# Kernel optimization log

Measured on AMD Instinct MI355X. Metric: run time of the kernel, lower is better.

Reference implementation:

```python
import jax, jax.numpy as jnp
import numpy as np

B, S, D, H = 2, 2048, 2048, 16
HD = D // H          # head dim 128
R = 64               # qk_rope_head_dim
LR = 64              # kv_low_rank_dim
FF = 2048            # ffn_dim per expert
E = 8                # num routed experts
K = 2                # top_k
ROPE_BASE = 10000.0
LN_EPS = 1e-5


def setup_inputs() -> dict:
    key = jax.random.key(0)
    ks = jax.random.split(key, 20)
    def rn(k, shape, fan_in):
        return jax.random.normal(k, shape, jnp.float32) * (1.0 / np.sqrt(fan_in))
    return {
        "hidden_states": jax.random.normal(ks[0], (B, S, D), jnp.float32),
        "position_ids": jnp.arange(S, dtype=jnp.int32)[None, :],
        # attention projections, stored [in, out]
        "Wq": rn(ks[1], (D, D), D), "Wk": rn(ks[2], (D, D), D), "Wv": rn(ks[3], (D, D), D),
        "Wkc": rn(ks[4], (HD, LR), HD), "Wvc": rn(ks[5], (HD, LR), HD),
        "Wqa": rn(ks[6], (HD, LR), HD), "Wqg": rn(ks[7], (HD, HD), HD),
        "Wov": rn(ks[8], (LR, HD), LR), "Wo": rn(ks[9], (D, D), D),
        "ln1_w": jnp.ones((D,), jnp.float32), "ln1_b": jnp.zeros((D,), jnp.float32),
        "ln2_w": jnp.ones((D,), jnp.float32), "ln2_b": jnp.zeros((D,), jnp.float32),
        # MoE
        "Wg": rn(ks[10], (D, E), D),
        "We1": rn(ks[11], (E, D, FF), D), "We2": rn(ks[12], (E, FF, D), FF), "We3": rn(ks[13], (E, D, FF), D),
        "Ws1": rn(ks[14], (D, FF), D), "Ws2": rn(ks[15], (FF, D), FF), "Ws3": rn(ks[16], (D, FF), D),
    }


def _layernorm(x, w, b):
    mu = jnp.mean(x, -1, keepdims=True)
    var = jnp.mean(jnp.square(x - mu), -1, keepdims=True)
    return (x - mu) * jax.lax.rsqrt(var + LN_EPS) * w + b


def _rotate_half(x):
    h = x.shape[-1] // 2
    return jnp.concatenate([-x[..., h:], x[..., :h]], axis=-1)


def _rope_cos_sin(position_ids, dtype):
    inv_freq = 1.0 / (ROPE_BASE ** (jnp.arange(0, R, 2, dtype=jnp.float32) / R))
    t = jnp.arange(S, dtype=jnp.float32)
    freqs = t[:, None] * inv_freq[None, :]           # [S, R/2]
    emb = jnp.concatenate([freqs, freqs], -1)        # [S, R]
    cos = jnp.cos(emb).astype(dtype)[position_ids][:, :, None, :]  # [1,S,1,R]
    sin = jnp.sin(emb).astype(dtype)[position_ids][:, :, None, :]
    return cos, sin


def reference(hidden_states, position_ids, Wq, Wk, Wv, Wkc, Wvc, Wqa, Wqg, Wov, Wo,
              ln1_w, ln1_b, ln2_w, ln2_b, Wg, We1, We2, We3, Ws1, Ws2, Ws3):
    x = _layernorm(hidden_states, ln1_w, ln1_b)
    # ---- MLA attention ----
    q = (x @ Wq).reshape(B, S, H, HD)
    k = (x @ Wk).reshape(B, S, H, HD)
    v = (x @ Wv).reshape(B, S, H, HD)
    cos, sin = _rope_cos_sin(position_ids, x.dtype)
    qr = q[..., :R] * cos + _rotate_half(q[..., :R]) * sin
    kr = k[..., :R] * cos + _rotate_half(k[..., :R]) * sin
    q = jnp.concatenate([qr, q[..., R:]], -1)
    k = jnp.concatenate([kr, k[..., R:]], -1)
    k_c = k @ Wkc                                   # [B,S,H,LR]
    v_c = v @ Wvc                                   # [B,S,H,LR]
    q_a = q @ Wqa                                   # [B,S,H,LR]
    q_gate = q @ Wqg                                # [B,S,H,HD]
    scores = jnp.einsum('bqhr,bkhr->bhqk', q_a, k_c) / np.sqrt(LR)
    attw = jax.nn.softmax(scores.astype(jnp.float32), axis=-1).astype(q.dtype)
    att_c = jnp.einsum('bhqk,bkhr->bqhr', attw, v_c)  # [B,S,H,LR]
    uplift = att_c @ Wov                              # [B,S,H,HD]
    gated = (jax.nn.silu(q_gate) * uplift).reshape(B, S, D)
    attn_out = gated @ Wo
    h = hidden_states + attn_out
    # ---- MoE with shared expert ----
    xf = _layernorm(h, ln2_w, ln2_b).reshape(-1, D)   # [T, D]
    shared = (jax.nn.silu(xf @ Ws1) * (xf @ Ws3)) @ Ws2
    logits = xf @ Wg                                  # [T, E]
    probs = jax.nn.softmax(logits.astype(jnp.float32), axis=-1)
    topw, topi = jax.lax.top_k(probs, K)
    topw = topw / jnp.sum(topw, -1, keepdims=True)
    T = xf.shape[0]
    combine = jnp.zeros((T, E), xf.dtype).at[jnp.arange(T)[:, None], topi].set(topw.astype(xf.dtype))
    h1 = jnp.einsum('td,edf->etf', xf, We1)
    h3 = jnp.einsum('td,edf->etf', xf, We3)
    eout = jnp.einsum('etf,efd->etd', jax.nn.silu(h1) * h3, We2)
    moe = shared + jnp.einsum('te,etd->td', combine, eout)
    return h + moe.reshape(B, S, D)
```

## Files before the change

### kernel.cpp

```cpp
#include <hip/hip_runtime.h>
#include <math.h>

typedef __bf16 bf16;
typedef __bf16 bf16x8 __attribute__((ext_vector_type(8)));
typedef float f32x4 __attribute__((ext_vector_type(4)));

#define B_ 2
#define S_ 2048
#define D_ 2048
#define H_ 16
#define FF_ 2048
#define E_ 8
#define T_ 4096
#define TH_ 65536
#define CAP_ 4096

#define MFMA_(a, b, c) __builtin_amdgcn_mfma_f32_16x16x32_bf16(a, b, c, 0, 0, 0)

__device__ __forceinline__ int swz(int row, int byteoff) {
  return row * 128 + (byteoff ^ ((row & 7) << 4));
}
__device__ __forceinline__ int swzf(int row, int byteoff) {
  return row * 256 + (byteoff ^ ((row & 7) << 5));
}

__device__ __forceinline__ void split2(float x, bf16& h, bf16& m) {
  h = (bf16)x;
  m = (bf16)(x - (float)h);
}

__device__ __forceinline__ void frag_split(const char* p, int off, bf16x8& r0, bf16x8& r1) {
  f32x4 u = *(const f32x4*)(p + off);
  f32x4 v = *(const f32x4*)(p + off + 16);
#pragma unroll
  for (int j = 0; j < 4; j++) { bf16 a, b; split2(u[j], a, b); r0[j] = a; r1[j] = b; }
#pragma unroll
  for (int j = 0; j < 4; j++) { bf16 a, b; split2(v[j], a, b); r0[4 + j] = a; r1[4 + j] = b; }
}

__device__ __forceinline__ f32x4 dot3(bf16x8 a0, bf16x8 a1,
                                      bf16x8 b0, bf16x8 b1, f32x4 c) {
  c = MFMA_(a0, b0, c);
  c = MFMA_(a0, b1, c);
  c = MFMA_(a1, b0, c);
  return c;
}

__device__ __forceinline__ float blk_sum(float v, float* sbuf, int tid) {
#pragma unroll
  for (int mk = 32; mk; mk >>= 1) v += __shfl_xor(v, mk);
  __syncthreads();
  if ((tid & 63) == 0) sbuf[tid >> 6] = v;
  __syncthreads();
  return sbuf[0] + sbuf[1] + sbuf[2] + sbuf[3];
}

__global__ __launch_bounds__(256) void k_transpose32(const float* __restrict__ src,
                                                     float* __restrict__ dst, int R, int C) {
  __shared__ float tile[32][33];
  int tx = threadIdx.x, ty = threadIdx.y;
  int c0 = blockIdx.x * 32, r0 = blockIdx.y * 32;
#pragma unroll
  for (int j = 0; j < 32; j += 8) tile[ty + j][tx] = src[(size_t)(r0 + ty + j) * C + (c0 + tx)];
  __syncthreads();
#pragma unroll
  for (int j = 0; j < 32; j += 8)
    dst[(size_t)(c0 + ty + j) * R + (r0 + tx)] = tile[tx][ty + j];
}

__global__ __launch_bounds__(256) void k_transpose32b3(const float* __restrict__ s0,
                                                       const float* __restrict__ s1x,
                                                       const float* __restrict__ s2,
                                                       float* __restrict__ dbase) {
  __shared__ float tile[32][33];
  int z = blockIdx.z;
  const float* src = z == 0 ? s0 : (z == 1 ? s1x : s2);
  float* dst = dbase + (size_t)z * 8192;
  int tx = threadIdx.x, ty = threadIdx.y;
  int c0 = blockIdx.x * 32, r0 = blockIdx.y * 32;
#pragma unroll
  for (int j = 0; j < 32; j += 8) tile[ty + j][tx] = src[(size_t)(r0 + ty + j) * 64 + (c0 + tx)];
  __syncthreads();
#pragma unroll
  for (int j = 0; j < 32; j += 8)
    dst[(size_t)(c0 + ty + j) * 128 + (r0 + tx)] = tile[tx][ty + j];
}

__global__ __launch_bounds__(256) void k_transpose_sh3(const float* __restrict__ s0,
                                                       const float* __restrict__ s1x,
                                                       const float* __restrict__ s2,
                                                       bf16* __restrict__ dbase) {
  __shared__ float tile[32][33];
  int z = blockIdx.z;
  const float* src = z == 0 ? s0 : (z == 1 ? s1x : s2);
  bf16* dst = dbase + (size_t)z * 4194304;
  int tx = threadIdx.x, ty = threadIdx.y;
  int c0 = blockIdx.x * 32, r0 = blockIdx.y * 32;
#pragma unroll
  for (int j = 0; j < 32; j += 8) tile[ty + j][tx] = src[(size_t)(r0 + ty + j) * 2048 + (c0 + tx)];
  __syncthreads();
#pragma unroll
  for (int j = 0; j < 32; j += 8)
    dst[(size_t)(c0 + ty + j) * 2048 + (r0 + tx)] = (bf16)tile[tx][ty + j];
}

template <int MODE>
__global__ __launch_bounds__(256) void k_transpose_moe(const float* __restrict__ W1,
                                                       const float* __restrict__ W3,
                                                       bf16* __restrict__ dstB, int eBase) {
  __shared__ float tile[32][33];
  int tx = threadIdx.x, ty = threadIdx.y;
  int z = blockIdx.z;
  const float* src;
  if (MODE == 0) src = ((z & 1) ? W3 : W1) + (size_t)(eBase + (z >> 1)) * 4194304;
  else src = W1 + (size_t)(eBase + z) * 4194304;
  bf16* dst = dstB + (size_t)z * 4194304;
  int c0 = blockIdx.x * 32, r0 = blockIdx.y * 32;
#pragma unroll
  for (int j = 0; j < 32; j += 8) tile[ty + j][tx] = src[(size_t)(r0 + ty + j) * 2048 + (c0 + tx)];
  __syncthreads();
#pragma unroll
  for (int j = 0; j < 32; j += 8)
    dst[(size_t)(c0 + ty + j) * 2048 + (r0 + tx)] = (bf16)tile[tx][ty + j];
}

__global__ __launch_bounds__(256) void k_transpose_split(const float* __restrict__ src,
                                                         bf16* __restrict__ dh, bf16* __restrict__ dl,
                                                         int R, int C) {
  __shared__ float tile[32][33];
  int tx = threadIdx.x, ty = threadIdx.y;
  int c0 = blockIdx.x * 32, r0 = blockIdx.y * 32;
#pragma unroll
  for (int j = 0; j < 32; j += 8) tile[ty + j][tx] = src[(size_t)(r0 + ty + j) * C + (c0 + tx)];
  __syncthreads();
#pragma unroll
  for (int j = 0; j < 32; j += 8) {
    float v = tile[tx][ty + j];
    bf16 h, l;
    split2(v, h, l);
    size_t o = (size_t)(c0 + ty + j) * R + (r0 + tx);
    dh[o] = h;
    dl[o] = l;
  }
}

__global__ __launch_bounds__(256) void k_transpose_split3(const float* __restrict__ s0,
                                                          const float* __restrict__ s1x,
                                                          const float* __restrict__ s2,
                                                          bf16* __restrict__ dbase) {
  __shared__ float tile[32][33];
  int z = blockIdx.z;
  const float* src = z == 0 ? s0 : (z == 1 ? s1x : s2);
  bf16* dh = dbase + (size_t)z * 8388608;
  bf16* dl = dh + 4194304;
  int tx = threadIdx.x, ty = threadIdx.y;
  int c0 = blockIdx.x * 32, r0 = blockIdx.y * 32;
#pragma unroll
  for (int j = 0; j < 32; j += 8) tile[ty + j][tx] = src[(size_t)(r0 + ty + j) * 2048 + (c0 + tx)];
  __syncthreads();
#pragma unroll
  for (int j = 0; j < 32; j += 8) {
    float v = tile[tx][ty + j];
    bf16 h, l;
    split2(v, h, l);
    size_t o = (size_t)(c0 + ty + j) * 2048 + (r0 + tx);
    dh[o] = h;
    dl[o] = l;
  }
}

__global__ __launch_bounds__(256) void k_tr_v32s(const float* __restrict__ vc,
                                                 bf16* __restrict__ vh, bf16* __restrict__ vl) {
  __shared__ float tile[32][33];
  int tx = threadIdx.x, ty = threadIdx.y;
  int z = blockIdx.z;
  int s0 = blockIdx.x * 32, r0 = blockIdx.y * 32;
  int b = z >> 4, h = z & 15;
#pragma unroll
  for (int j = 0; j < 32; j += 8) {
    int s = s0 + ty + j;
    tile[ty + j][tx] = vc[((size_t)((b * S_ + s) * H_ + h)) * 64 + r0 + tx];
  }
  __syncthreads();
#pragma unroll
  for (int j = 0; j < 32; j += 8) {
    int r = r0 + ty + j;
    float v = tile[tx][ty + j];
    bf16 hh, ll;
    split2(v, hh, ll);
    size_t o = ((size_t)(z * 64 + r)) * S_ + s0 + tx;
    vh[o] = hh;
    vl[o] = ll;
  }
}

__global__ __launch_bounds__(256) void k_ln32_split(const float* __restrict__ x, const float* __restrict__ w,
                                                    const float* __restrict__ bb,
                                                    bf16* __restrict__ oh, bf16* __restrict__ ol) {
  __shared__ float sbuf[4];
  int row = blockIdx.x, tid = threadIdx.x;
  const float* xr = x + (size_t)row * D_;
  float v[8];
  float s = 0.f;
#pragma unroll
  for (int j = 0; j < 8; j++) { v[j] = xr[tid + 256 * j]; s += v[j]; }
  float mu = blk_sum(s, sbuf, tid) * (1.f / D_);
  float qs = 0.f;
#pragma unroll
  for (int j = 0; j < 8; j++) { float d = v[j] - mu; qs += d * d; }
  float rs = rsqrtf(blk_sum(qs, sbuf, tid) * (1.f / D_) + 1e-5f);
#pragma unroll
  for (int j = 0; j < 8; j++) {
    int c = tid + 256 * j;
    float xn = (v[j] - mu) * rs * w[c] + bb[c];
    bf16 h, l;
    split2(xn, h, l);
    oh[(size_t)row * D_ + c] = h;
    ol[(size_t)row * D_ + c] = l;
  }
}

template <int EPI>
__global__ __launch_bounds__(256) void k_gemm32s(const bf16* __restrict__ Ah, const bf16* __restrict__ Al, int lda,
                                                 const bf16* __restrict__ Bh, const bf16* __restrict__ Bl, int ldb,
                                                 float* __restrict__ C, int ldc,
                                                 int M, int N, int Kd,
                                                 const float* __restrict__ resid) {
  __shared__ __align__(16) char Ahs[16384];
  __shared__ __align__(16) char Als[16384];
  __shared__ __align__(16) char Bhs[16384];
  __shared__ __align__(16) char Bls[16384];
  int bm = blockIdx.y * 128, bn = blockIdx.x * 128;
  int tid = threadIdx.x;
  int srow = tid >> 3, scol = (tid & 7) * 8;
  int arow[4], brow[4];
#pragma unroll
  for (int i = 0; i < 4; i++) {
    int r = bm + srow + 32 * i;
    arow[i] = r < M ? r : (M - 1);
    int q = bn + srow + 32 * i;
    brow[i] = q < N ? q : (N - 1);
  }
  f32x4 acc[4][4] = {};
  int lane = tid & 63, w = tid >> 6, g = lane >> 4, lr = lane & 15;
  int wm = (w >> 1) * 64, wn = (w & 1) * 64;
  for (int kt = 0; kt < Kd; kt += 64) {
#pragma unroll
    for (int i = 0; i < 4; i++) {
      int o = swz(srow + 32 * i, scol * 2);
      *(uint4*)(Ahs + o) = *(const uint4*)(Ah + (size_t)arow[i] * lda + kt + scol);
      *(uint4*)(Als + o) = *(const uint4*)(Al + (size_t)arow[i] * lda + kt + scol);
      *(uint4*)(Bhs + o) = *(const uint4*)(Bh + (size_t)brow[i] * ldb + kt + scol);
      *(uint4*)(Bls + o) = *(const uint4*)(Bl + (size_t)brow[i] * ldb + kt + scol);
    }
    __syncthreads();
#pragma unroll
    for (int ks = 0; ks < 2; ks++) {
      bf16x8 ah[4], al[4], bh[4], bl[4];
#pragma unroll
      for (int m = 0; m < 4; m++) {
        ah[m] = *(const bf16x8*)(Ahs + swz(wm + m * 16 + lr, ks * 64 + g * 16));
        al[m] = *(const bf16x8*)(Als + swz(wm + m * 16 + lr, ks * 64 + g * 16));
      }
#pragma unroll
      for (int n = 0; n < 4; n++) {
        bh[n] = *(const bf16x8*)(Bhs + swz(wn + n * 16 + lr, ks * 64 + g * 16));
        bl[n] = *(const bf16x8*)(Bls + swz(wn + n * 16 + lr, ks * 64 + g * 16));
      }
#pragma unroll
      for (int m = 0; m < 4; m++)
#pragma unroll
        for (int n = 0; n < 4; n++)
          acc[m][n] = dot3(ah[m], al[m], bh[n], bl[n], acc[m][n]);
    }
    __syncthreads();
  }
#pragma unroll
  for (int m = 0; m < 4; m++)
#pragma unroll
    for (int n = 0; n < 4; n++)
#pragma unroll
      for (int r = 0; r < 4; r++) {
        int row = bm + wm + m * 16 + g * 4 + r;
        int col = bn + wn + n * 16 + lr;
        if (row < M && col < N) {
          float val = acc[m][n][r];
          if (EPI == 1) val += resid[(size_t)row * ldc + col];
          C[(size_t)row * ldc + col] = val;
        }
      }
}

__global__ __launch_bounds__(256) void k_gemm32s_qkv(const bf16* __restrict__ Ah, const bf16* __restrict__ Al,
                                                     const bf16* __restrict__ Bhb,
                                                     float* __restrict__ Cb) {
  int z = blockIdx.z;
  const bf16* Bh = Bhb + (size_t)z * 8388608;
  const bf16* Bl = Bh + 4194304;
  float* C = Cb + (size_t)z * 8388608;
  __shared__ __align__(16) char Ahs[16384];
  __shared__ __align__(16) char Als[16384];
  __shared__ __align__(16) char Bhs[16384];
  __shared__ __align__(16) char Bls[16384];
  int bm = blockIdx.y * 128, bn = blockIdx.x * 128;
  int tid = threadIdx.x;
  int srow = tid >> 3, scol = (tid & 7) * 8;
  f32x4 acc[4][4] = {};
  int lane = tid & 63, w = tid >> 6, g = lane >> 4, lr = lane & 15;
  int wm = (w >> 1) * 64, wn = (w & 1) * 64;
  for (int kt = 0; kt < 2048; kt += 64) {
#pragma unroll
    for (int i = 0; i < 4; i++) {
      int row = srow + 32 * i;
      int o = swz(row, scol * 2);
      *(uint4*)(Ahs + o) = *(const uint4*)(Ah + (size_t)(bm + row) * 2048 + kt + scol);
      *(uint4*)(Als + o) = *(const uint4*)(Al + (size_t)(bm + row) * 2048 + kt + scol);
      *(uint4*)(Bhs + o) = *(const uint4*)(Bh + (size_t)(bn + row) * 2048 + kt + scol);
      *(uint4*)(Bls + o) = *(const uint4*)(Bl + (size_t)(bn + row) * 2048 + kt + scol);
    }
    __syncthreads();
#pragma unroll
    for (int ks = 0; ks < 2; ks++) {
      bf16x8 ah[4], al[4], bh[4], bl[4];
#pragma unroll
      for (int m = 0; m < 4; m++) {
        ah[m] = *(const bf16x8*)(Ahs + swz(wm + m * 16 + lr, ks * 64 + g * 16));
        al[m] = *(const bf16x8*)(Als + swz(wm + m * 16 + lr, ks * 64 + g * 16));
      }
#pragma unroll
      for (int n = 0; n < 4; n++) {
        bh[n] = *(const bf16x8*)(Bhs + swz(wn + n * 16 + lr, ks * 64 + g * 16));
        bl[n] = *(const bf16x8*)(Bls + swz(wn + n * 16 + lr, ks * 64 + g * 16));
      }
#pragma unroll
      for (int m = 0; m < 4; m++)
#pragma unroll
        for (int n = 0; n < 4; n++)
          acc[m][n] = dot3(ah[m], al[m], bh[n], bl[n], acc[m][n]);
    }
    __syncthreads();
  }
#pragma unroll
  for (int m = 0; m < 4; m++)
#pragma unroll
    for (int n = 0; n < 4; n++)
#pragma unroll
      for (int r = 0; r < 4; r++) {
        int row = bm + wm + m * 16 + g * 4 + r;
        int col = bn + wn + n * 16 + lr;
        C[(size_t)row * 2048 + col] = acc[m][n][r];
      }
}

template <int EPI>
__global__ __launch_bounds__(256) void k_gemm32(const float* __restrict__ A, int lda,
                                                const float* __restrict__ Bt, int ldb,
                                                float* __restrict__ C, int ldc,
                                                int M, int N, int Kd,
                                                bf16* __restrict__ Ch, bf16* __restrict__ Cl) {
  __shared__ __align__(16) char As[32768];
  __shared__ __align__(16) char Bs[32768];
  int bm = blockIdx.y * 128, bn = blockIdx.x * 128;
  int tid = threadIdx.x;
  int srow = tid >> 3, scol = (tid & 7) * 8;
  int arow[4], brow[4];
#pragma unroll
  for (int i = 0; i < 4; i++) {
    int r = bm + srow + 32 * i;
    arow[i] = r < M ? r : (M - 1);
    int q = bn + srow + 32 * i;
    brow[i] = q < N ? q : (N - 1);
  }
  f32x4 acc[4][4] = {};
  int lane = tid & 63, w = tid >> 6, g = lane >> 4, lr = lane & 15;
  int wm = (w >> 1) * 64, wn = (w & 1) * 64;
  for (int kt = 0; kt < Kd; kt += 64) {
#pragma unroll
    for (int i = 0; i < 4; i++) {
      const float* pa = A + (size_t)arow[i] * lda + kt + scol;
      f32x4 va0 = *(const f32x4*)pa, va1 = *(const f32x4*)(pa + 4);
      const float* pb = Bt + (size_t)brow[i] * ldb + kt + scol;
      f32x4 vb0 = *(const f32x4*)pb, vb1 = *(const f32x4*)(pb + 4);
      int o = swzf(srow + 32 * i, scol * 4);
      *(f32x4*)(As + o) = va0;
      *(f32x4*)(As + o + 16) = va1;
      *(f32x4*)(Bs + o) = vb0;
      *(f32x4*)(Bs + o + 16) = vb1;
    }
    __syncthreads();
#pragma unroll
    for (int ks = 0; ks < 2; ks++) {
      bf16x8 a0[4], a1[4], b0[4], b1[4];
#pragma unroll
      for (int m = 0; m < 4; m++)
        frag_split(As, swzf(wm + m * 16 + lr, ks * 128 + g * 32), a0[m], a1[m]);
#pragma unroll
      for (int n = 0; n < 4; n++)
        frag_split(Bs, swzf(wn + n * 16 + lr, ks * 128 + g * 32), b0[n], b1[n]);
#pragma unroll
      for (int m = 0; m < 4; m++)
#pragma unroll
        for (int n = 0; n < 4; n++)
          acc[m][n] = dot3(a0[m], a1[m], b0[n], b1[n], acc[m][n]);
    }
    __syncthreads();
  }
#pragma unroll
  for (int m = 0; m < 4; m++)
#pragma unroll
    for (int n = 0; n < 4; n++)
#pragma unroll
      for (int r = 0; r < 4; r++) {
        int row = bm + wm + m * 16 + g * 4 + r;
        int col = bn + wn + n * 16 + lr;
        if (row < M && col < N) {
          C[(size_t)row * ldc + col] = acc[m][n][r];
        }
      }
}

__global__ __launch_bounds__(256) void k_projn64(const float* __restrict__ Ab,
                                                 const float* __restrict__ Btb,
                                                 bf16* __restrict__ Pb,
                                                 float* __restrict__ Vb) {
  int z = blockIdx.z;
  const float* A = Ab + (size_t)z * 8388608;
  const float* Bt = Btb + (size_t)z * 8192;
  __shared__ __align__(16) char As[32768];
  __shared__ __align__(16) char Bs[16384];
  int bm = blockIdx.y * 128;
  int tid = threadIdx.x;
  int lane = tid & 63, w = tid >> 6, g = lane >> 4, lr = lane & 15;
  int arowB = tid >> 2;
  int acol = (tid & 3) * 16;
  f32x4 acc[2][4] = {};
  for (int kt = 0; kt < 128; kt += 64) {
#pragma unroll
    for (int i = 0; i < 2; i++) {
      int row = arowB + 64 * i;
      const float* pa = A + (size_t)(bm + row) * 128 + kt + acol;
#pragma unroll
      for (int j = 0; j < 4; j++)
        *(f32x4*)(As + swzf(row, (acol + j * 4) * 4)) = *(const f32x4*)(pa + j * 4);
    }
    {
      const float* pb = Bt + (size_t)arowB * 128 + kt + acol;
#pragma unroll
      for (int j = 0; j < 4; j++)
        *(f32x4*)(Bs + swzf(arowB, (acol + j * 4) * 4)) = *(const f32x4*)(pb + j * 4);
    }
    __syncthreads();
#pragma unroll
    for (int ks = 0; ks < 2; ks++) {
      bf16x8 a0[2], a1[2], b0[4], b1[4];
#pragma unroll
      for (int m = 0; m < 2; m++)
        frag_split(As, swzf(w * 32 + m * 16 + lr, ks * 128 + g * 32), a0[m], a1[m]);
#pragma unroll
      for (int n = 0; n < 4; n++)
        frag_split(Bs, swzf(n * 16 + lr, ks * 128 + g * 32), b0[n], b1[n]);
#pragma unroll
      for (int m = 0; m < 2; m++)
#pragma unroll
        for (int n = 0; n < 4; n++)
          acc[m][n] = dot3(a0[m], a1[m], b0[n], b1[n], acc[m][n]);
    }
    __syncthreads();
  }
  bf16* Ph = Pb + (size_t)z * 8388608;
  bf16* Pl = Ph + 4194304;
#pragma unroll
  for (int m = 0; m < 2; m++)
#pragma unroll
    for (int n = 0; n < 4; n++)
#pragma unroll
      for (int r = 0; r < 4; r++) {
        int row = bm + w * 32 + m * 16 + g * 4 + r;
        int col = n * 16 + lr;
        size_t o = (size_t)row * 64 + col;
        float val = acc[m][n][r];
        if (z == 2) {
          Vb[o] = val;
        } else {
          bf16 h, l;
          split2(val, h, l);
          Ph[o] = h;
          Pl[o] = l;
        }
      }
}

__global__ __launch_bounds__(256) void k_rope32(float* __restrict__ q, float* __restrict__ k) {
  int idx = blockIdx.x * 256 + threadIdx.x;
  int i = idx & 31, rowth = idx >> 5;
  int s = (rowth >> 4) & (S_ - 1);
  size_t base = (size_t)rowth * 128;
  float freq = expf(-0.28782313662425576f * (float)i);
  float ang = (float)s * freq;
  float sn, cs;
  sincosf(ang, &sn, &cs);
  float q1 = q[base + i], q2 = q[base + i + 32];
  q[base + i] = q1 * cs - q2 * sn;
  q[base + i + 32] = q2 * cs + q1 * sn;
  float k1 = k[base + i], k2 = k[base + i + 32];
  k[base + i] = k1 * cs - k2 * sn;
  k[base + i + 32] = k2 * cs + k1 * sn;
}

__global__ __launch_bounds__(256) void k_attn32p(const bf16* __restrict__ qh, const bf16* __restrict__ ql,
                                                 const bf16* __restrict__ kh, const bf16* __restrict__ kl,
                                                 const bf16* __restrict__ vh, const bf16* __restrict__ vl,
                                                 float* __restrict__ attc) {
  __shared__ __align__(16) char L[65536];
  int lin = blockIdx.x + 16 * blockIdx.y;
  int xcd = lin & 7, j = lin >> 3;
  int bh = xcd * 4 + (j & 3);
  int qt = j >> 2;
  int b = bh >> 4, h = bh & 15;
  int tid = threadIdx.x, lane = tid & 63, w = tid >> 6, g = lane >> 4, lr = lane & 15;
  int s0 = qt * 128;
  int srow = tid >> 3, scol = (tid & 7) * 8;
  char* Qsh = L;
  char* Qsl = L + 16384;
#pragma unroll
  for (int i = 0; i < 4; i++) {
    int row = srow + 32 * i;
    size_t goff = ((size_t)((b * S_ + s0 + row) * H_ + h)) * 64 + scol;
    int o = swz(row, scol * 2);
    *(uint4*)(Qsh + o) = *(const uint4*)(qh + goff);
    *(uint4*)(Qsl + o) = *(const uint4*)(ql + goff);
  }
  __syncthreads();
  bf16x8 qf0[2][2], qf1[2][2];
#pragma unroll
  for (int m = 0; m < 2; m++)
#pragma unroll
    for (int ks = 0; ks < 2; ks++) {
      qf0[m][ks] = *(const bf16x8*)(Qsh + swz(w * 32 + m * 16 + lr, ks * 64 + g * 16));
      qf1[m][ks] = *(const bf16x8*)(Qsl + swz(w * 32 + m * 16 + lr, ks * 64 + g * 16));
    }
  __syncthreads();
  char* Ksh = L;
  char* Ksl = L + 8192;
  char* Vsh = L + 16384;
  char* Vsl = L + 24576;
  char* Ph = L + 32768 + w * 8192;
  char* Pl = Ph + 4096;
  f32x4 acc[2][4] = {};
  float mrun[2][4], lrun[2][4];
#pragma unroll
  for (int m = 0; m < 2; m++)
#pragma unroll
    for (int r = 0; r < 4; r++) { mrun[m][r] = -1e30f; lrun[m][r] = 0.f; }
  for (int kt = 0; kt < S_; kt += 64) {
#pragma unroll
    for (int i = 0; i < 2; i++) {
      int rr = srow + 32 * i;
      size_t koff = ((size_t)((b * S_ + kt + rr) * H_ + h)) * 64 + scol;
      size_t voff = ((size_t)(bh * 64 + rr)) * S_ + kt + scol;
      int o = swz(rr, scol * 2);
      *(uint4*)(Ksh + o) = *(const uint4*)(kh + koff);
      *(uint4*)(Ksl + o) = *(const uint4*)(kl + koff);
      *(uint4*)(Vsh + o) = *(const uint4*)(vh + voff);
      *(uint4*)(Vsl + o) = *(const uint4*)(vl + voff);
    }
    __syncthreads();
    f32x4 sc[2][4] = {};
#pragma unroll
    for (int ks = 0; ks < 2; ks++) {
      bf16x8 k0[4], k1[4];
#pragma unroll
      for (int n = 0; n < 4; n++) {
        k0[n] = *(const bf16x8*)(Ksh + swz(n * 16 + lr, ks * 64 + g * 16));
        k1[n] = *(const bf16x8*)(Ksl + swz(n * 16 + lr, ks * 64 + g * 16));
      }
      __builtin_amdgcn_s_setprio(1);
#pragma unroll
      for (int m = 0; m < 2; m++)
#pragma unroll
        for (int n = 0; n < 4; n++)
          sc[m][n] = dot3(qf0[m][ks], qf1[m][ks], k0[n], k1[n], sc[m][n]);
      __builtin_amdgcn_s_setprio(0);
    }
#pragma unroll
    for (int m = 0; m < 2; m++)
#pragma unroll
      for (int r = 0; r < 4; r++) {
        float a0 = sc[m][0][r] * 0.125f, a1 = sc[m][1][r] * 0.125f;
        float a2 = sc[m][2][r] * 0.125f, a3 = sc[m][3][r] * 0.125f;
        float mx = fmaxf(fmaxf(a0, a1), fmaxf(a2, a3));
#pragma unroll
        for (int mk = 1; mk < 16; mk <<= 1) mx = fmaxf(mx, __shfl_xor(mx, mk));
        float mo = mrun[m][r];
        float mn = fmaxf(mo, mx);
        float f = expf(mo - mn);
        float p0 = expf(a0 - mn), p1 = expf(a1 - mn), p2 = expf(a2 - mn), p3 = expf(a3 - mn);
        int prow = m * 16 + g * 4 + r;
        bf16 h0, l0, h1, l1, h2, l2, h3, l3;
        split2(p0, h0, l0);
        split2(p1, h1, l1);
        split2(p2, h2, l2);
        split2(p3, h3, l3);
        *(bf16*)(Ph + swz(prow, lr * 2)) = h0;
        *(bf16*)(Pl + swz(prow, lr * 2)) = l0;
        *(bf16*)(Ph + swz(prow, 32 + lr * 2)) = h1;
        *(bf16*)(Pl + swz(prow, 32 + lr * 2)) = l1;
        *(bf16*)(Ph + swz(prow, 64 + lr * 2)) = h2;
        *(bf16*)(Pl + swz(prow, 64 + lr * 2)) = l2;
        *(bf16*)(Ph + swz(prow, 96 + lr * 2)) = h3;
        *(bf16*)(Pl + swz(prow, 96 + lr * 2)) = l3;
        float ps = p0 + p1 + p2 + p3;
#pragma unroll
        for (int mk = 1; mk < 16; mk <<= 1) ps += __shfl_xor(ps, mk);
        lrun[m][r] = lrun[m][r] * f + ps;
        mrun[m][r] = mn;
#pragma unroll
        for (int n = 0; n < 4; n++) acc[m][n][r] *= f;
      }
#pragma unroll
    for (int ks = 0; ks < 2; ks++) {
      bf16x8 p0f[2], p1f[2], v0f[4], v1f[4];
#pragma unroll
      for (int m = 0; m < 2; m++) {
        p0f[m] = *(const bf16x8*)(Ph + swz(m * 16 + lr, ks * 64 + g * 16));
        p1f[m] = *(const bf16x8*)(Pl + swz(m * 16 + lr, ks * 64 + g * 16));
      }
#pragma unroll
      for (int n = 0; n < 4; n++) {
        v0f[n] = *(const bf16x8*)(Vsh + swz(n * 16 + lr, ks * 64 + g * 16));
        v1f[n] = *(const bf16x8*)(Vsl + swz(n * 16 + lr, ks * 64 + g * 16));
      }
      __builtin_amdgcn_s_setprio(1);
#pragma unroll
      for (int m = 0; m < 2; m++)
#pragma unroll
        for (int n = 0; n < 4; n++)
          acc[m][n] = dot3(p0f[m], p1f[m], v0f[n], v1f[n], acc[m][n]);
      __builtin_amdgcn_s_setprio(0);
    }
    __syncthreads();
  }
#pragma unroll
  for (int m = 0; m < 2; m++)
#pragma unroll
    for (int n = 0; n < 4; n++)
#pragma unroll
      for (int r = 0; r < 4; r++) {
        int s = s0 + w * 32 + m * 16 + g * 4 + r;
        attc[((size_t)((b * S_ + s) * H_ + h)) * 64 + n * 16 + lr] = acc[m][n][r] / lrun[m][r];
      }
}

__global__ __launch_bounds__(256) void k_silu32_split(const float* __restrict__ a, const float* __restrict__ b,
                                                      bf16* __restrict__ ch, bf16* __restrict__ cl, long n) {
  long i = ((long)blockIdx.x * 256 + threadIdx.x) * 8;
  if (i >= n) return;
  f32x4 av0 = *(const f32x4*)(a + i), av1 = *(const f32x4*)(a + i + 4);
  f32x4 bv0 = *(const f32x4*)(b + i), bv1 = *(const f32x4*)(b + i + 4);
  bf16x8 hv, lv;
#pragma unroll
  for (int j = 0; j < 4; j++) {
    float x = av0[j];
    float g = x / (1.f + expf(-x)) * bv0[j];
    bf16 h, l;
    split2(g, h, l);
    hv[j] = h; lv[j] = l;
  }
#pragma unroll
  for (int j = 0; j < 4; j++) {
    float x = av1[j];
    float g = x / (1.f + expf(-x)) * bv1[j];
    bf16 h, l;
    split2(g, h, l);
    hv[4 + j] = h; lv[4 + j] = l;
  }
  *(bf16x8*)(ch + i) = hv;
  *(bf16x8*)(cl + i) = lv;
}

__global__ __launch_bounds__(256) void k_router(const float* __restrict__ hbuf,
                                                const float* __restrict__ w2, const float* __restrict__ b2,
                                                const float* __restrict__ Wg, bf16* __restrict__ xf,
                                                int* __restrict__ count, int* __restrict__ permg,
                                                int* __restrict__ permt, float* __restrict__ wslot) {
  __shared__ float sbuf[4];
  int t = blockIdx.x, tid = threadIdx.x;
  const float* hr = hbuf + (size_t)t * D_;
  float v[8];
  float s = 0.f;
#pragma unroll
  for (int j = 0; j < 8; j++) { v[j] = hr[tid + 256 * j]; s += v[j]; }
  float mu = blk_sum(s, sbuf, tid) * (1.f / D_);
  float qs = 0.f;
#pragma unroll
  for (int j = 0; j < 8; j++) { float d = v[j] - mu; qs += d * d; }
  float rs = rsqrtf(blk_sum(qs, sbuf, tid) * (1.f / D_) + 1e-5f);
  float le[8] = {0, 0, 0, 0, 0, 0, 0, 0};
#pragma unroll
  for (int j = 0; j < 8; j++) {
    int c = tid + 256 * j;
    float xn = (v[j] - mu) * rs * w2[c] + b2[c];
    xf[(size_t)t * D_ + c] = (bf16)xn;
    const float* wr = Wg + (size_t)c * 8;
#pragma unroll
    for (int e = 0; e < 8; e++) le[e] += xn * wr[e];
  }
#pragma unroll
  for (int e = 0; e < 8; e++) le[e] = blk_sum(le[e], sbuf, tid);
  if (tid == 0) {
    float mx = le[0];
    for (int e = 1; e < 8; e++) mx = fmaxf(mx, le[e]);
    float p[8], sum = 0.f;
    for (int e = 0; e < 8; e++) { p[e] = expf(le[e] - mx); sum += p[e]; }
    int i0 = 0;
    for (int e = 1; e < 8; e++) if (p[e] > p[i0]) i0 = e;
    int i1 = (i0 == 0) ? 1 : 0;
    for (int e = 0; e < 8; e++) if (e != i0 && p[e] > p[i1]) i1 = e;
    float inv = 1.f / (p[i0] + p[i1]);
    int pos0 = atomicAdd(&count[i0], 1);
    permg[i0 * CAP_ + pos0] = 2 * t;
    permt[i0 * CAP_ + pos0] = t;
    int pos1 = atomicAdd(&count[i1], 1);
    permg[i1 * CAP_ + pos1] = 2 * t + 1;
    permt[i1 * CAP_ + pos1] = t;
    wslot[2 * t] = p[i0] * inv;
    wslot[2 * t + 1] = p[i1] * inv;
  }
}

template <bool GATHER>
__global__ __launch_bounds__(256) void k_gemm(const bf16* __restrict__ A, int lda,
                                              const bf16* __restrict__ Bt, int ldb,
                                              bf16* __restrict__ C, int ldc, int M, int N, int Kd,
                                              const int* __restrict__ amap,
                                              const int* __restrict__ cmap,
                                              const int* __restrict__ countp) {
  int Mz = countp ? countp[0] : M;
  int bm = blockIdx.y * 128, bn = blockIdx.x * 128;
  if (bm >= Mz) return;
  __shared__ __align__(16) char As[16384];
  __shared__ __align__(16) char Bs[16384];
  int tid = threadIdx.x;
  int srow = tid >> 3, scol = (tid & 7) * 8;
  int arow[4], brow[4];
#pragma unroll
  for (int i = 0; i < 4; i++) {
    int r = bm + srow + 32 * i;
    if (GATHER) { int rc = r < Mz ? r : (Mz - 1); arow[i] = amap[rc]; }
    else { arow[i] = r < M ? r : (M - 1); }
    int bq = bn + srow + 32 * i;
    brow[i] = bq < N ? bq : (N - 1);
  }
  f32x4 acc[4][4] = {};
  int lane = tid & 63, w = tid >> 6, g = lane >> 4, lr = lane & 15;
  int wm = (w >> 1) * 64, wn = (w & 1) * 64;
  for (int kt = 0; kt < Kd; kt += 64) {
#pragma unroll
    for (int i = 0; i < 4; i++) {
      uint4 da = *(const uint4*)(A + (size_t)arow[i] * lda + kt + scol);
      *(uint4*)(As + swz(srow + 32 * i, scol * 2)) = da;
      uint4 db = *(const uint4*)(Bt + (size_t)brow[i] * ldb + kt + scol);
      *(uint4*)(Bs + swz(srow + 32 * i, scol * 2)) = db;
    }
    __syncthreads();
#pragma unroll
    for (int ks = 0; ks < 2; ks++) {
      bf16x8 af[4], bfr[4];
#pragma unroll
      for (int m = 0; m < 4; m++) af[m] = *(const bf16x8*)(As + swz(wm + m * 16 + lr, ks * 64 + g * 16));
#pragma unroll
      for (int n = 0; n < 4; n++) bfr[n] = *(const bf16x8*)(Bs + swz(wn + n * 16 + lr, ks * 64 + g * 16));
#pragma unroll
      for (int m = 0; m < 4; m++)
#pragma unroll
        for (int n = 0; n < 4; n++)
          acc[m][n] = MFMA_(af[m], bfr[n], acc[m][n]);
    }
    __syncthreads();
  }
#pragma unroll
  for (int m = 0; m < 4; m++)
#pragma unroll
    for (int n = 0; n < 4; n++)
#pragma unroll
      for (int r = 0; r < 4; r++) {
        int row = bm + wm + m * 16 + g * 4 + r;
        int col = bn + wn + n * 16 + lr;
        if (row < Mz && col < N) {
          size_t orow = cmap ? (size_t)cmap[row] : (size_t)row;
          C[orow * ldc + col] = (bf16)acc[m][n][r];
        }
      }
}

template <int MODE>
__global__ __launch_bounds__(256) void k_gemm_moe(const bf16* __restrict__ A, int lda,
                                                  const bf16* __restrict__ wteB,
                                                  bf16* __restrict__ C0, bf16* __restrict__ C1, int ldc,
                                                  int N, int Kd,
                                                  const int* __restrict__ permt, const int* __restrict__ permg,
                                                  const int* __restrict__ count, int eBase) {
  int z = blockIdx.z;
  int e;
  const int* amap;
  const int* cmap;
  bf16* C;
  if (MODE == 0) {
    e = eBase + (z >> 1);
    amap = permt + e * CAP_;
    cmap = permg + e * CAP_;
    C = (z & 1) ? C1 : C0;
  } else {
    e = eBase + z;
    amap = permg + e * CAP_;
    cmap = permg + e * CAP_;
    C = C0;
  }
  const bf16* Bt = wteB + (size_t)z * 4194304;
  int Mz = count[e];
  int bm = blockIdx.y * 128, bn = blockIdx.x * 128;
  if (bm >= Mz) return;
  __shared__ __align__(16) char As[16384];
  __shared__ __align__(16) char Bs[16384];
  int tid = threadIdx.x;
  int srow = tid >> 3, scol = (tid & 7) * 8;
  int arow[4], brow[4];
#pragma unroll
  for (int i = 0; i < 4; i++) {
    int r = bm + srow + 32 * i;
    int rc = r < Mz ? r : (Mz - 1);
    arow[i] = amap[rc];
    int bq = bn + srow + 32 * i;
    brow[i] = bq < N ? bq : (N - 1);
  }
  f32x4 acc[4][4] = {};
  int lane = tid & 63, w = tid >> 6, g = lane >> 4, lr = lane & 15;
  int wm = (w >> 1) * 64, wn = (w & 1) * 64;
  for (int kt = 0; kt < Kd; kt += 64) {
#pragma unroll
    for (int i = 0; i < 4; i++) {
      uint4 da = *(const uint4*)(A + (size_t)arow[i] * lda + kt + scol);
      *(uint4*)(As + swz(srow + 32 * i, scol * 2)) = da;
      uint4 db = *(const uint4*)(Bt + (size_t)brow[i] * 2048 + kt + scol);
      *(uint4*)(Bs + swz(srow + 32 * i, scol * 2)) = db;
    }
    __syncthreads();
#pragma unroll
    for (int ks = 0; ks < 2; ks++) {
      bf16x8 af[4], bfr[4];
#pragma unroll
      for (int m = 0; m < 4; m++) af[m] = *(const bf16x8*)(As + swz(wm + m * 16 + lr, ks * 64 + g * 16));
#pragma unroll
      for (int n = 0; n < 4; n++) bfr[n] = *(const bf16x8*)(Bs + swz(wn + n * 16 + lr, ks * 64 + g * 16));
#pragma unroll
      for (int m = 0; m < 4; m++)
#pragma unroll
        for (int n = 0; n < 4; n++)
          acc[m][n] = MFMA_(af[m], bfr[n], acc[m][n]);
    }
    __syncthreads();
  }
#pragma unroll
  for (int m = 0; m < 4; m++)
#pragma unroll
    for (int n = 0; n < 4; n++)
#pragma unroll
      for (int r = 0; r < 4; r++) {
        int row = bm + wm + m * 16 + g * 4 + r;
        int col = bn + wn + n * 16 + lr;
        if (row < Mz && col < N) {
          C[(size_t)cmap[row] * ldc + col] = (bf16)acc[m][n][r];
        }
      }
}

__global__ __launch_bounds__(256) void k_silu_mul(const bf16* __restrict__ a, const bf16* __restrict__ b,
                                                  bf16* __restrict__ c, long n) {
  long i = ((long)blockIdx.x * 256 + threadIdx.x) * 8;
  if (i >= n) return;
  bf16x8 av = *(const bf16x8*)(a + i);
  bf16x8 bv = *(const bf16x8*)(b + i);
  bf16x8 cv;
#pragma unroll
  for (int j = 0; j < 8; j++) {
    float x = (float)av[j];
    float y = (float)bv[j];
    cv[j] = (bf16)(x / (1.f + expf(-x)) * y);
  }
  *(bf16x8*)(c + i) = cv;
}

__global__ __launch_bounds__(256) void k_combine(const float* __restrict__ hbuf, const bf16* __restrict__ shr,
                                                 const bf16* __restrict__ eout, const float* __restrict__ wslot,
                                                 float* __restrict__ out) {
  long i = ((long)blockIdx.x * 256 + threadIdx.x) * 4;
  int t = (int)(i >> 11);
  int c = (int)(i & (D_ - 1));
  float w0 = wslot[2 * t], w1 = wslot[2 * t + 1];
  float4 hv = *(const float4*)(hbuf + i);
  const bf16* s4 = shr + i;
  const bf16* e0 = eout + ((size_t)(2 * t)) * D_ + c;
  const bf16* e1 = e0 + D_;
  float4 o;
  o.x = hv.x + (float)s4[0] + w0 * (float)e0[0] + w1 * (float)e1[0];
  o.y = hv.y + (float)s4[1] + w0 * (float)e0[1] + w1 * (float)e1[1];
  o.z = hv.z + (float)s4[2] + w0 * (float)e0[2] + w1 * (float)e1[2];
  o.w = hv.w + (float)s4[3] + w0 * (float)e0[3] + w1 * (float)e1[3];
  *(float4*)(out + i) = o;
}

extern "C" void kernel_launch(void* const* d_in, const int* in_sizes, int n_in, void* d_out,
                              int out_size, void* d_ws, size_t ws_size, hipStream_t stream) {
  const float* hidden = (const float*)d_in[0];
  const float* Wq = (const float*)d_in[2];
  const float* Wk = (const float*)d_in[3];
  const float* Wv = (const float*)d_in[4];
  const float* Wkc = (const float*)d_in[5];
  const float* Wvc = (const float*)d_in[6];
  const float* Wqa = (const float*)d_in[7];
  const float* Wqg = (const float*)d_in[8];
  const float* Wov = (const float*)d_in[9];
  const float* Wo = (const float*)d_in[10];
  const float* ln1w = (const float*)d_in[11];
  const float* ln1b = (const float*)d_in[12];
  const float* ln2w = (const float*)d_in[13];
  const float* ln2b = (const float*)d_in[14];
  const float* Wg = (const float*)d_in[15];
  const float* We1 = (const float*)d_in[16];
  const float* We2 = (const float*)d_in[17];
  const float* We3 = (const float*)d_in[18];
  const float* Ws1 = (const float*)d_in[19];
  const float* Ws2 = (const float*)d_in[20];
  const float* Ws3 = (const float*)d_in[21];
  float* out = (float*)d_out;
  (void)in_sizes; (void)n_in; (void)out_size;

  const size_t MB = 1ull << 20;
  char* base = (char*)d_ws;
  float* hbuf = (float*)(base);
  bf16* shr = (bf16*)(base + 32 * MB);
  int* count = (int*)(base + 48 * MB);
  int* permg = (int*)(base + 48 * MB + 4096);
  int* permt = (int*)(base + 48 * MB + 4096 + 131072);
  float* wslot = (float*)(base + 48 * MB + 4096 + 262144);
  float* wtqa32 = (float*)(base + 49 * MB);
  float* wtov32 = (float*)(base + 49 * MB + 98304);
  float* wtqg32 = (float*)(base + 49 * MB + 131072);
  char* A0p = base + 50 * MB;
  char* A1p = base + 82 * MB;
  char* A2p = base + 114 * MB;
  char* A3p = base + 146 * MB;
  char* A4p = base + 178 * MB;
  char* A5p = base + 210 * MB;
  if (ws_size < 242 * MB) return;

  bf16* xln_h = (bf16*)A0p;
  bf16* xln_l = (bf16*)(A0p + 16 * MB);
  bf16* wtqkv = (bf16*)A1p;
  float* qb = (float*)A3p;
  float* kb = (float*)A4p;
  float* vb = (float*)A5p;
  bf16* qab_h = (bf16*)A1p;
  bf16* qab_l = (bf16*)(A1p + 8 * MB);
  bf16* kcb_h = (bf16*)(A1p + 16 * MB);
  bf16* kcb_l = (bf16*)(A1p + 24 * MB);
  float* vcb = (float*)A2p;
  bf16* vct_h = (bf16*)(A2p + 16 * MB);
  bf16* vct_l = (bf16*)(A2p + 24 * MB);
  float* qgate = (float*)A0p;
  float* attc = (float*)A3p;
  bf16* wto_h = (bf16*)(A3p + 16 * MB);
  bf16* wto_l = (bf16*)(A3p + 24 * MB);
  float* uplift = (float*)A4p;
  bf16* gated_h = (bf16*)A5p;
  bf16* gated_l = (bf16*)(A5p + 16 * MB);
  bf16* xf = (bf16*)A1p;
  bf16* s1 = (bf16*)(A1p + 16 * MB);
  bf16* wts1 = (bf16*)A2p;
  bf16* wts3 = (bf16*)(A2p + 8 * MB);
  bf16* wts2 = (bf16*)(A2p + 16 * MB);
  bf16* s3 = (bf16*)A3p;
  bf16* wteB_mid = (bf16*)A2p;
  bf16* wteB_out = (bf16*)A1p;
  bf16* mid1 = (bf16*)A4p;
  bf16* mid3 = (bf16*)A5p;
  bf16* midg = (bf16*)A0p;
  bf16* eout = (bf16*)A3p;

  hipMemsetAsync(count, 0, 256, stream);

  dim3 tb(32, 8);
  k_transpose_split3<<<dim3(64, 64, 3), tb, 0, stream>>>(Wq, Wk, Wv, wtqkv);
  k_transpose32b3<<<dim3(2, 4, 3), tb, 0, stream>>>(Wqa, Wkc, Wvc, wtqa32);
  k_transpose32<<<dim3(4, 4, 1), tb, 0, stream>>>(Wqg, wtqg32, 128, 128);
  k_transpose32<<<dim3(4, 2, 1), tb, 0, stream>>>(Wov, wtov32, 64, 128);

  k_ln32_split<<<T_, 256, 0, stream>>>(hidden, ln1w, ln1b, xln_h, xln_l);

  k_gemm32s_qkv<<<dim3(16, 32, 3), 256, 0, stream>>>(xln_h, xln_l, wtqkv, qb);

  k_rope32<<<8192, 256, 0, stream>>>(qb, kb);

  k_projn64<<<dim3(1, 512, 3), 256, 0, stream>>>(qb, wtqa32, qab_h, vcb);
  k_gemm32<0><<<dim3(1, 512, 1), 256, 0, stream>>>(qb, 128, wtqg32, 128, qgate, 128, TH_, 128, 128, nullptr, nullptr);

  k_tr_v32s<<<dim3(64, 2, 32), tb, 0, stream>>>(vcb, vct_h, vct_l);
  k_transpose_split<<<dim3(64, 64, 1), tb, 0, stream>>>(Wo, wto_h, wto_l, 2048, 2048);

  k_attn32p<<<dim3(16, 32, 1), 256, 0, stream>>>(qab_h, qab_l, kcb_h, kcb_l, vct_h, vct_l, attc);

  k_transpose_sh3<<<dim3(64, 64, 3), tb, 0, stream>>>(Ws1, Ws3, Ws2, wts1);

  k_gemm32<0><<<dim3(1, 512, 1), 256, 0, stream>>>(attc, 64, wtov32, 64, uplift, 128, TH_, 128, 64, nullptr, nullptr);
  k_silu32_split<<<4096, 256, 0, stream>>>(qgate, uplift, gated_h, gated_l, (long)TH_ * 128);
  k_gemm32s<1><<<dim3(16, 32, 1), 256, 0, stream>>>(gated_h, gated_l, 2048, wto_h, wto_l, 2048, hbuf, 2048, T_, 2048, 2048, hidden);

  k_router<<<T_, 256, 0, stream>>>(hbuf, ln2w, ln2b, Wg, xf, count, permg, permt, wslot);

  k_gemm<false><<<dim3(16, 32, 1), 256, 0, stream>>>(xf, 2048, wts1, 2048, s1, 2048, T_, 2048, 2048, nullptr, nullptr, nullptr);
  k_gemm<false><<<dim3(16, 32, 1), 256, 0, stream>>>(xf, 2048, wts3, 2048, s3, 2048, T_, 2048, 2048, nullptr, nullptr, nullptr);
  k_silu_mul<<<4096, 256, 0, stream>>>(s1, s3, s1, (long)T_ * 2048);
  k_gemm<false><<<dim3(16, 32, 1), 256, 0, stream>>>(s1, 2048, wts2, 2048, shr, 2048, T_, 2048, 2048, nullptr, nullptr, nullptr);

  for (int p = 0; p < 2; p++) {
    k_transpose_moe<0><<<dim3(64, 64, 8), tb, 0, stream>>>(We1, We3, wteB_mid, 4 * p);
    k_gemm_moe<0><<<dim3(16, 32, 8), 256, 0, stream>>>(xf, 2048, wteB_mid, mid1, mid3, 2048, 2048, 2048, permt, permg, count, 4 * p);
  }
  k_silu_mul<<<8192, 256, 0, stream>>>(mid1, mid3, midg, (long)2 * T_ * 2048);
  k_transpose_moe<1><<<dim3(64, 64, 8), tb, 0, stream>>>(We2, nullptr, wteB_out, 0);
  k_gemm_moe<1><<<dim3(16, 32, 8), 256, 0, stream>>>(midg, 2048, wteB_out, eout, nullptr, 2048, 2048, 2048, permt, permg, count, 0);

  k_combine<<<8192, 256, 0, stream>>>(hbuf, shr, eout, wslot, out);
}
```

Baseline: 1.612 ms.

## Fuse RoPE into QKV GEMM epilogue and batch shared-expert GEMMs with MoE launches

RoPE is now applied in the QKV projection GEMM epilogue instead of a separate pass over q and k. The shared-expert W1/W3 GEMMs run as one two-slice launch. The shared W2 down-projection and its weight transpose are merged into the MoE down-projection launches as an extra z-slice. The aim is fewer launches, less memory traffic and better GPU fill, at the cost of rearranged buffer aliasing and sincos work in the GEMM epilogue.

```diff
diff --git a/kernel.cpp b/kernel.cpp
--- a/kernel.cpp
+++ b/kernel.cpp
@@ -104,17 +104,32 @@
     dst[(size_t)(c0 + ty + j) * 2048 + (r0 + tx)] = (bf16)tile[tx][ty + j];
 }
 
-template <int MODE>
 __global__ __launch_bounds__(256) void k_transpose_moe(const float* __restrict__ W1,
                                                        const float* __restrict__ W3,
                                                        bf16* __restrict__ dstB, int eBase) {
   __shared__ float tile[32][33];
   int tx = threadIdx.x, ty = threadIdx.y;
   int z = blockIdx.z;
-  const float* src;
-  if (MODE == 0) src = ((z & 1) ? W3 : W1) + (size_t)(eBase + (z >> 1)) * 4194304;
-  else src = W1 + (size_t)(eBase + z) * 4194304;
+  const float* src = ((z & 1) ? W3 : W1) + (size_t)(eBase + (z >> 1)) * 4194304;
   bf16* dst = dstB + (size_t)z * 4194304;
+  int c0 = blockIdx.x * 32, r0 = blockIdx.y * 32;
+#pragma unroll
+  for (int j = 0; j < 32; j += 8) tile[ty + j][tx] = src[(size_t)(r0 + ty + j) * 2048 + (c0 + tx)];
+  __syncthreads();
+#pragma unroll
+  for (int j = 0; j < 32; j += 8)
+    dst[(size_t)(c0 + ty + j) * 2048 + (r0 + tx)] = (bf16)tile[tx][ty + j];
+}
+
+__global__ __launch_bounds__(256) void k_transpose_moe2(const float* __restrict__ We2,
+                                                        const float* __restrict__ Ws2,
+                                                        bf16* __restrict__ dstB,
+                                                        bf16* __restrict__ dst2) {
+  __shared__ float tile[32][33];
+  int tx = threadIdx.x, ty = threadIdx.y;
+  int z = blockIdx.z;
+  const float* src = (z < 8) ? (We2 + (size_t)z * 4194304) : Ws2;
+  bf16* dst = (z < 8) ? (dstB + (size_t)z * 4194304) : dst2;
   int c0 = blockIdx.x * 32, r0 = blockIdx.y * 32;
 #pragma unroll
   for (int j = 0; j < 32; j += 8) tile[ty + j][tx] = src[(size_t)(r0 + ty + j) * 2048 + (c0 + tx)];
@@ -340,6 +355,26 @@
     }
     __syncthreads();
   }
+  if (z < 2 && wn == 0) {
+#pragma unroll
+    for (int n = 0; n < 2; n++) {
+      float fi = (float)(n * 16 + lr);
+      float freq = expf(-0.28782313662425576f * fi);
+#pragma unroll
+      for (int m = 0; m < 4; m++)
+#pragma unroll
+        for (int r = 0; r < 4; r++) {
+          int row = bm + wm + m * 16 + g * 4 + r;
+          int s = row & (S_ - 1);
+          float ang = (float)s * freq;
+          float sn, cs;
+          sincosf(ang, &sn, &cs);
+          float q1 = acc[m][n][r], q2 = acc[m][n + 2][r];
+          acc[m][n][r] = q1 * cs - q2 * sn;
+          acc[m][n + 2][r] = q2 * cs + q1 * sn;
+        }
+    }
+  }
 #pragma unroll
   for (int m = 0; m < 4; m++)
 #pragma unroll
@@ -488,23 +523,6 @@
           Pl[o] = l;
         }
       }
-}
-
-__global__ __launch_bounds__(256) void k_rope32(float* __restrict__ q, float* __restrict__ k) {
-  int idx = blockIdx.x * 256 + threadIdx.x;
-  int i = idx & 31, rowth = idx >> 5;
-  int s = (rowth >> 4) & (S_ - 1);
-  size_t base = (size_t)rowth * 128;
-  float freq = expf(-0.28782313662425576f * (float)i);
-  float ang = (float)s * freq;
-  float sn, cs;
-  sincosf(ang, &sn, &cs);
-  float q1 = q[base + i], q2 = q[base + i + 32];
-  q[base + i] = q1 * cs - q2 * sn;
-  q[base + i + 32] = q2 * cs + q1 * sn;
-  float k1 = k[base + i], k2 = k[base + i + 32];
-  k[base + i] = k1 * cs - k2 * sn;
-  k[base + i + 32] = k2 * cs + k1 * sn;
 }
 
 __global__ __launch_bounds__(256) void k_attn32p(const bf16* __restrict__ qh, const bf16* __restrict__ ql,
@@ -728,39 +746,28 @@
   }
 }
 
-template <bool GATHER>
-__global__ __launch_bounds__(256) void k_gemm(const bf16* __restrict__ A, int lda,
-                                              const bf16* __restrict__ Bt, int ldb,
-                                              bf16* __restrict__ C, int ldc, int M, int N, int Kd,
-                                              const int* __restrict__ amap,
-                                              const int* __restrict__ cmap,
-                                              const int* __restrict__ countp) {
-  int Mz = countp ? countp[0] : M;
-  int bm = blockIdx.y * 128, bn = blockIdx.x * 128;
-  if (bm >= Mz) return;
+__global__ __launch_bounds__(256) void k_gemm_sh(const bf16* __restrict__ A,
+                                                 const bf16* __restrict__ Bt0, const bf16* __restrict__ Bt1,
+                                                 bf16* __restrict__ C0, bf16* __restrict__ C1) {
+  int z = blockIdx.z;
+  const bf16* Bt = z ? Bt1 : Bt0;
+  bf16* C = z ? C1 : C0;
   __shared__ __align__(16) char As[16384];
   __shared__ __align__(16) char Bs[16384];
+  int bm = blockIdx.y * 128, bn = blockIdx.x * 128;
   int tid = threadIdx.x;
   int srow = tid >> 3, scol = (tid & 7) * 8;
-  int arow[4], brow[4];
-#pragma unroll
-  for (int i = 0; i < 4; i++) {
-    int r = bm + srow + 32 * i;
-    if (GATHER) { int rc = r < Mz ? r : (Mz - 1); arow[i] = amap[rc]; }
-    else { arow[i] = r < M ? r : (M - 1); }
-    int bq = bn + srow + 32 * i;
-    brow[i] = bq < N ? bq : (N - 1);
-  }
   f32x4 acc[4][4] = {};
   int lane = tid & 63, w = tid >> 6, g = lane >> 4, lr = lane & 15;
   int wm = (w >> 1) * 64, wn = (w & 1) * 64;
-  for (int kt = 0; kt < Kd; kt += 64) {
+  for (int kt = 0; kt < 2048; kt += 64) {
 #pragma unroll
     for (int i = 0; i < 4; i++) {
-      uint4 da = *(const uint4*)(A + (size_t)arow[i] * lda + kt + scol);
-      *(uint4*)(As + swz(srow + 32 * i, scol * 2)) = da;
-      uint4 db = *(const uint4*)(Bt + (size_t)brow[i] * ldb + kt + scol);
-      *(uint4*)(Bs + swz(srow + 32 * i, scol * 2)) = db;
+      int row = srow + 32 * i;
+      uint4 da = *(const uint4*)(A + (size_t)(bm + row) * 2048 + kt + scol);
+      *(uint4*)(As + swz(row, scol * 2)) = da;
+      uint4 db = *(const uint4*)(Bt + (size_t)(bn + row) * 2048 + kt + scol);
+      *(uint4*)(Bs + swz(row, scol * 2)) = db;
     }
     __syncthreads();
 #pragma unroll
@@ -786,14 +793,10 @@
       for (int r = 0; r < 4; r++) {
         int row = bm + wm + m * 16 + g * 4 + r;
         int col = bn + wn + n * 16 + lr;
-        if (row < Mz && col < N) {
-          size_t orow = cmap ? (size_t)cmap[row] : (size_t)row;
-          C[orow * ldc + col] = (bf16)acc[m][n][r];
-        }
-      }
-}
-
-template <int MODE>
+        C[(size_t)row * 2048 + col] = (bf16)acc[m][n][r];
+      }
+}
+
 __global__ __launch_bounds__(256) void k_gemm_moe(const bf16* __restrict__ A, int lda,
                                                   const bf16* __restrict__ wteB,
                                                   bf16* __restrict__ C0, bf16* __restrict__ C1, int ldc,
@@ -801,21 +804,10 @@
                                                   const int* __restrict__ permt, const int* __restrict__ permg,
                                                   const int* __restrict__ count, int eBase) {
   int z = blockIdx.z;
-  int e;
-  const int* amap;
-  const int* cmap;
-  bf16* C;
-  if (MODE == 0) {
-    e = eBase + (z >> 1);
-    amap = permt + e * CAP_;
-    cmap = permg + e * CAP_;
-    C = (z & 1) ? C1 : C0;
-  } else {
-    e = eBase + z;
-    amap = permg + e * CAP_;
-    cmap = permg + e * CAP_;
-    C = C0;
-  }
+  int e = eBase + (z >> 1);
+  const int* amap = permt + e * CAP_;
+  const int* cmap = permg + e * CAP_;
+  bf16* C = (z & 1) ? C1 : C0;
   const bf16* Bt = wteB + (size_t)z * 4194304;
   int Mz = count[e];
   int bm = blockIdx.y * 128, bn = blockIdx.x * 128;
@@ -870,6 +862,88 @@
         int col = bn + wn + n * 16 + lr;
         if (row < Mz && col < N) {
           C[(size_t)cmap[row] * ldc + col] = (bf16)acc[m][n][r];
+        }
+      }
+}
+
+__global__ __launch_bounds__(256) void k_gemm_moe_dn(const bf16* __restrict__ Amoe,
+                                                     const bf16* __restrict__ Ash,
+                                                     const bf16* __restrict__ wteB,
+                                                     const bf16* __restrict__ wts2t,
+                                                     bf16* __restrict__ Ce, bf16* __restrict__ Cs,
+                                                     const int* __restrict__ permg,
+                                                     const int* __restrict__ count) {
+  int z = blockIdx.z;
+  const bf16* A;
+  const bf16* Bt;
+  bf16* C;
+  const int* map = nullptr;
+  int Mz;
+  if (z < 8) {
+    A = Amoe;
+    Bt = wteB + (size_t)z * 4194304;
+    C = Ce;
+    map = permg + z * CAP_;
+    Mz = count[z];
+  } else {
+    A = Ash;
+    Bt = wts2t;
+    C = Cs;
+    Mz = T_;
+  }
+  int bm = blockIdx.y * 128, bn = blockIdx.x * 128;
+  if (bm >= Mz) return;
+  __shared__ __align__(16) char As[16384];
+  __shared__ __align__(16) char Bs[16384];
+  int tid = threadIdx.x;
+  int srow = tid >> 3, scol = (tid & 7) * 8;
+  int arow[4], brow[4];
+#pragma unroll
+  for (int i = 0; i < 4; i++) {
+    int r = bm + srow + 32 * i;
+    int rc = r < Mz ? r : (Mz - 1);
+    arow[i] = map ? map[rc] : rc;
+    int bq = bn + srow + 32 * i;
+    brow[i] = bq;
+  }
+  f32x4 acc[4][4] = {};
+  int lane = tid & 63, w = tid >> 6, g = lane >> 4, lr = lane & 15;
+  int wm = (w >> 1) * 64, wn = (w & 1) * 64;
+  for (int kt = 0; kt < 2048; kt += 64) {
+#pragma unroll
+    for (int i = 0; i < 4; i++) {
+      uint4 da = *(const uint4*)(A + (size_t)arow[i] * 2048 + kt + scol);
+      *(uint4*)(As + swz(srow + 32 * i, scol * 2)) = da;
+      uint4 db = *(const uint4*)(Bt + (size_t)brow[i] * 2048 + kt + scol);
+      *(uint4*)(Bs + swz(srow + 32 * i, scol * 2)) = db;
+    }
+    __syncthreads();
+#pragma unroll
+    for (int ks = 0; ks < 2; ks++) {
+      bf16x8 af[4], bfr[4];
+#pragma unroll
+      for (int m = 0; m < 4; m++) af[m] = *(const bf16x8*)(As + swz(wm + m * 16 + lr, ks * 64 + g * 16));
+#pragma unroll
+      for (int n = 0; n < 4; n++) bfr[n] = *(const bf16x8*)(Bs + swz(wn + n * 16 + lr, ks * 64 + g * 16));
+#pragma unroll
+      for (int m = 0; m < 4; m++)
+#pragma unroll
+        for (int n = 0; n < 4; n++)
+          acc[m][n] = MFMA_(af[m], bfr[n], acc[m][n]);
+    }
+    __syncthreads();
+  }
+#pragma unroll
+  for (int m = 0; m < 4; m++)
+#pragma unroll
+    for (int n = 0; n < 4; n++)
+#pragma unroll
+      for (int r = 0; r < 4; r++) {
+        int row = bm + wm + m * 16 + g * 4 + r;
+        int col = bn + wn + n * 16 + lr;
+        if (row < Mz) {
+          size_t orow = map ? (size_t)map[row] : (size_t)row;
+          C[orow * 2048 + col] = (bf16)acc[m][n][r];
         }
       }
 }
@@ -958,8 +1032,6 @@
   bf16* xln_l = (bf16*)(A0p + 16 * MB);
   bf16* wtqkv = (bf16*)A1p;
   float* qb = (float*)A3p;
-  float* kb = (float*)A4p;
-  float* vb = (float*)A5p;
   bf16* qab_h = (bf16*)A1p;
   bf16* qab_l = (bf16*)(A1p + 8 * MB);
   bf16* kcb_h = (bf16*)(A1p + 16 * MB);
@@ -978,14 +1050,14 @@
   bf16* s1 = (bf16*)(A1p + 16 * MB);
   bf16* wts1 = (bf16*)A2p;
   bf16* wts3 = (bf16*)(A2p + 8 * MB);
-  bf16* wts2 = (bf16*)(A2p + 16 * MB);
   bf16* s3 = (bf16*)A3p;
   bf16* wteB_mid = (bf16*)A2p;
-  bf16* wteB_out = (bf16*)A1p;
+  bf16* wteB_dn = (bf16*)A2p;
+  bf16* wts2t = (bf16*)A1p;
   bf16* mid1 = (bf16*)A4p;
   bf16* mid3 = (bf16*)A5p;
   bf16* midg = (bf16*)A0p;
-  bf16* eout = (bf16*)A3p;
+  bf16* eout = (bf16*)A4p;
 
   hipMemsetAsync(count, 0, 256, stream);
 
@@ -999,8 +1071,6 @@
 
   k_gemm32s_qkv<<<dim3(16, 32, 3), 256, 0, stream>>>(xln_h, xln_l, wtqkv, qb);
 
-  k_rope32<<<8192, 256, 0, stream>>>(qb, kb);
-
   k_projn64<<<dim3(1, 512, 3), 256, 0, stream>>>(qb, wtqa32, qab_h, vcb);
   k_gemm32<0><<<dim3(1, 512, 1), 256, 0, stream>>>(qb, 128, wtqg32, 128, qgate, 128, TH_, 128, 128, nullptr, nullptr);
 
@@ -1017,18 +1087,17 @@
 
   k_router<<<T_, 256, 0, stream>>>(hbuf, ln2w, ln2b, Wg, xf, count, permg, permt, wslot);
 
-  k_gemm<false><<<dim3(16, 32, 1), 256, 0, stream>>>(xf, 2048, wts1, 2048, s1, 2048, T_, 2048, 2048, nullptr, nullptr, nullptr);
-  k_gemm<false><<<dim3(16, 32, 1), 256, 0, stream>>>(xf, 2048, wts3, 2048, s3, 2048, T_, 2048, 2048, nullptr, nullptr, nullptr);
+  k_gemm_sh<<<dim3(16, 32, 2), 256, 0, stream>>>(xf, wts1, wts3, s1, s3);
   k_silu_mul<<<4096, 256, 0, stream>>>(s1, s3, s1, (long)T_ * 2048);
-  k_gemm<false><<<dim3(16, 32, 1), 256, 0, stream>>>(s1, 2048, wts2, 2048, shr, 2048, T_, 2048, 2048, nullptr, nullptr, nullptr);
 
   for (int p = 0; p < 2; p++) {
-    k_transpose_moe<0><<<dim3(64, 64, 8), tb, 0, stream>>>(We1, We3, wteB_mid, 4 * p);
-    k_gemm_moe<0><<<dim3(16, 32, 8), 256, 0, stream>>>(xf, 2048, wteB_mid, mid1, mid3, 2048, 2048, 2048, permt, permg, count, 4 * p);
+    k_transpose_moe<<<dim3(64, 64, 8), tb, 0, stream>>>(We1, We3, wteB_mid, 4 * p);
+    k_gemm_moe<<<dim3(16, 32, 8), 256, 0, stream>>>(xf, 2048, wteB_mid, mid1, mid3, 2048, 2048, 2048, permt, permg, count, 4 * p);
   }
   k_silu_mul<<<8192, 256, 0, stream>>>(mid1, mid3, midg, (long)2 * T_ * 2048);
-  k_transpose_moe<1><<<dim3(64, 64, 8), tb, 0, stream>>>(We2, nullptr, wteB_out, 0);
-  k_gemm_moe<1><<<dim3(16, 32, 8), 256, 0, stream>>>(midg, 2048, wteB_out, eout, nullptr, 2048, 2048, 2048, permt, permg, count, 0);
+
+  k_transpose_moe2<<<dim3(64, 64, 9), tb, 0, stream>>>(We2, Ws2, wteB_dn, wts2t);
+  k_gemm_moe_dn<<<dim3(16, 32, 9), 256, 0, stream>>>(midg, s1, wteB_dn, wts2t, eout, shr, permg, count);
 
   k_combine<<<8192, 256, 0, stream>>>(hbuf, shr, eout, wslot, out);
 }
```

Measured after the change: 1.743 ms. 8.1% more time.
